# Kernel tuning notes

Measured on AMD Instinct MI355X. Metric: run time of the kernel, lower is better.

## Reference

```python
import jax, jax.numpy as jnp
import numpy as np

B_GRAPHS = 16      # number of graphs in batch
NPG = 8192         # nodes per graph
N = B_GRAPHS * NPG # 131072 total nodes
F_DIM = 64         # node feature dim
K_CLUST = 16       # n_clusters
DEG = 32           # avg degree
E = N * DEG        # 4,194,304 edges


def setup_inputs() -> dict:
    key = jax.random.key(0)
    k1, k2, k3, k4, k5 = jax.random.split(key, 5)
    x = jax.random.normal(k1, (N, F_DIM), jnp.float32)
    W = jax.random.normal(k2, (F_DIM, K_CLUST), jnp.float32) / np.sqrt(F_DIM)
    b = jnp.zeros((K_CLUST,), jnp.float32)
    # edges constrained within each graph -> block-diagonal adjacency (PyG batching)
    g = jnp.repeat(jnp.arange(B_GRAPHS, dtype=jnp.int32), E // B_GRAPHS)
    edge_row = g * NPG + jax.random.randint(k3, (E,), 0, NPG, jnp.int32)
    edge_col = g * NPG + jax.random.randint(k4, (E,), 0, NPG, jnp.int32)
    edge_weight = jax.random.uniform(k5, (E,), jnp.float32)
    return {"x": x, "W": W, "b": b, "edge_weight": edge_weight,
            "edge_row": edge_row, "edge_col": edge_col, "num_graphs": B_GRAPHS}


def _forward(x, W, b, edge_weight, edge_row, edge_col, num_graphs):
    Ntot, Fd = x.shape
    K = W.shape[1]
    Bn = num_graphs
    n = Ntot // Bn  # equal-size graphs (ptr = n * arange(B+1))

    s = x @ W + b                                   # [N,K] cluster logits
    xb = x.reshape(Bn, n, Fd)
    sb = s.reshape(Bn, n, K)
    # out_x = selu(s^T @ x_bd), block b = s_b^T x_b, then hsplit_and_vstack -> [B*K, F]
    out_x = jax.nn.selu(jnp.einsum('bnk,bnf->bkf', sb, xb)).reshape(Bn * K, Fd)

    ss = jax.nn.softmax(s, axis=-1)                 # softmaxed assignments
    ssb = ss.reshape(Bn, n, K)

    # degree d = adj.sum(axis=0)  (column sums over COO edges)
    d = jax.ops.segment_sum(edge_weight, edge_col, num_segments=Ntot)   # [N]
    m2 = d.reshape(Bn, n).sum(1)                    # total degree per graph [B]

    # A @ C via edge scatter: (A C)[row] += w * C[col]
    AC = jax.ops.segment_sum(edge_weight[:, None] * ss[edge_col], edge_row,
                             num_segments=Ntot)     # [N,K]
    # out_adj blocks: C_b^T A_b C_b  -> [B,K,K]
    out_adj = jnp.einsum('bnk,bnl->bkl', ssb, AC.reshape(Bn, n, K))

    # dS_b = C_b^T d_b  (Ca/Cb blocks); normalizer gets m_inv twice in torch code
    dS = jnp.einsum('bn,bnk->bk', d.reshape(Bn, n), ssb)                # [B,K]
    spectral_loss = -jnp.mean(jnp.einsum('bkk->b', out_adj) / m2
                              - (dS ** 2).sum(1) / (m2 ** 2))

    sqrt_K = jnp.sqrt(jnp.float32(K))
    cluster_size = ssb.sum(1)                        # [B,K]
    cluster_loss = jnp.mean(jnp.sqrt((cluster_size ** 2).sum(1)) / n * sqrt_K - 1.0)

    # CC blocks: C_b^T C_b; ortho = mean_b || CC_b/||CC_b||_F - I/sqrt(K) ||_F
    CC = jnp.einsum('bnk,bnl->bkl', ssb, ssb)        # [B,K,K]
    CC_norm = jnp.sqrt((CC ** 2).sum((1, 2)))        # Frobenius norm per block
    eye_div_k = jnp.eye(K, dtype=x.dtype) / sqrt_K
    ortho_loss = jnp.mean(jnp.sqrt(
        ((CC / CC_norm[:, None, None] - eye_div_k) ** 2).sum((1, 2))))

    # mask diagonal and degree-normalize pooled adjacency
    oa = out_adj * (1.0 - jnp.eye(K, dtype=x.dtype))
    dd = jnp.sqrt(oa.sum(2)) + 1e-12                 # row sums per block [B,K]
    out_adj_norm = oa / (dd[:, :, None] * dd[:, None, :])

    return out_x, out_adj_norm, spectral_loss, cluster_loss, ortho_loss


def reference(x, W, b, edge_weight, edge_row, edge_col, num_graphs):
    return _forward(x, W, b, edge_weight, edge_row, edge_col, num_graphs)
```

## Files before the change

### kernel.cpp

```cpp
#include <hip/hip_runtime.h>
#include <math.h>

#define F_DIM 64
#define K_CL 16
#define B_GR 16
#define SROW 72

typedef _Float16 h16;
using f16x4 = __attribute__((ext_vector_type(4))) _Float16;
using f16x8 = __attribute__((ext_vector_type(8))) _Float16;
using f32x4 = __attribute__((ext_vector_type(4))) float;
using fx2   = __attribute__((ext_vector_type(2))) float;
using fp16x2 = __attribute__((ext_vector_type(2))) __fp16;

static __device__ inline unsigned h2u(fp16x2 h) {
    union { fp16x2 h; unsigned u; } x; x.h = h; return x.u;
}

__global__ __launch_bounds__(256) void k_fused(
    const float* __restrict__ x, const float* __restrict__ W, const float* __restrict__ bvec,
    uint4* __restrict__ ssh8, float* __restrict__ outx, float* __restrict__ CCb)
{
    __shared__ float Wl[F_DIM * K_CL];
    __shared__ float bl[K_CL];
    __shared__ __align__(16) h16 stage[4][(16 + 16 + 64) * SROW];

    int t = threadIdx.x;
    for (int idx = t; idx < F_DIM * K_CL; idx += 256) Wl[idx] = W[idx];
    if (t < K_CL) bl[t] = bvec[t];
    __syncthreads();

    int wid = t >> 6, lane = t & 63;
    h16* Sg = stage[wid];
    h16* Cg = Sg + 16 * SROW;
    h16* Xg = Cg + 16 * SROW;

    size_t i = (size_t)blockIdx.x * 256 + t;
    float s[16];
#pragma unroll
    for (int k = 0; k < 16; ++k) s[k] = bl[k];

    const float4* xp = reinterpret_cast<const float4*>(x + i * F_DIM);
#pragma unroll
    for (int j = 0; j < 16; ++j) {
        float4 q = xp[j];
        float xf[4] = {q.x, q.y, q.z, q.w};
#pragma unroll
        for (int ff = 0; ff < 4; ++ff) {
            int f = j * 4 + ff;
            float xv = xf[ff];
            Xg[f * SROW + lane] = (h16)xv;
            const float4* wr = reinterpret_cast<const float4*>(&Wl[f * K_CL]);
            float4 w0 = wr[0], w1 = wr[1], w2 = wr[2], w3 = wr[3];
            s[0]  += xv * w0.x; s[1]  += xv * w0.y; s[2]  += xv * w0.z; s[3]  += xv * w0.w;
            s[4]  += xv * w1.x; s[5]  += xv * w1.y; s[6]  += xv * w1.z; s[7]  += xv * w1.w;
            s[8]  += xv * w2.x; s[9]  += xv * w2.y; s[10] += xv * w2.z; s[11] += xv * w2.w;
            s[12] += xv * w3.x; s[13] += xv * w3.y; s[14] += xv * w3.z; s[15] += xv * w3.w;
        }
    }

#pragma unroll
    for (int k = 0; k < 16; ++k) Sg[k * SROW + lane] = (h16)s[k];

    float m = s[0];
#pragma unroll
    for (int k = 1; k < 16; ++k) m = fmaxf(m, s[k]);
    float sum = 0.f;
#pragma unroll
    for (int k = 0; k < 16; ++k) { s[k] = __expf(s[k] - m); sum += s[k]; }
    float inv = 1.0f / sum;
#pragma unroll
    for (int k = 0; k < 16; ++k) s[k] *= inv;

    f16x8 h0, h1;
#pragma unroll
    for (int k = 0; k < 8; ++k) { h0[k] = (h16)s[k]; h1[k] = (h16)s[k + 8]; }
#pragma unroll
    for (int k = 0; k < 8; ++k) {
        Cg[k * SROW + lane] = h0[k];
        Cg[(k + 8) * SROW + lane] = h1[k];
    }

    {
        unsigned d0, d1, d2, d3;
        d0 = __builtin_amdgcn_cvt_pk_fp8_f32(s[0],  s[1],  0,  false);
        d0 = __builtin_amdgcn_cvt_pk_fp8_f32(s[2],  s[3],  d0, true);
        d1 = __builtin_amdgcn_cvt_pk_fp8_f32(s[4],  s[5],  0,  false);
        d1 = __builtin_amdgcn_cvt_pk_fp8_f32(s[6],  s[7],  d1, true);
        d2 = __builtin_amdgcn_cvt_pk_fp8_f32(s[8],  s[9],  0,  false);
        d2 = __builtin_amdgcn_cvt_pk_fp8_f32(s[10], s[11], d2, true);
        d3 = __builtin_amdgcn_cvt_pk_fp8_f32(s[12], s[13], 0,  false);
        d3 = __builtin_amdgcn_cvt_pk_fp8_f32(s[14], s[15], d3, true);
        uint4 pk; pk.x = d0; pk.y = d1; pk.z = d2; pk.w = d3;
        ssh8[i] = pk;
    }

    int q4 = lane >> 4, mm = lane & 15;
    f32x4 accO[4] = {{0.f,0.f,0.f,0.f},{0.f,0.f,0.f,0.f},{0.f,0.f,0.f,0.f},{0.f,0.f,0.f,0.f}};
    f32x4 accC = {0.f, 0.f, 0.f, 0.f};
#pragma unroll
    for (int h = 0; h < 2; ++h) {
        f16x8 aO = *(const f16x8*)&Sg[mm * SROW + h * 32 + q4 * 8];
        f16x8 aC = *(const f16x8*)&Cg[mm * SROW + h * 32 + q4 * 8];
        accC = __builtin_amdgcn_mfma_f32_16x16x32_f16(aC, aC, accC, 0, 0, 0);
#pragma unroll
        for (int ft = 0; ft < 4; ++ft) {
            f16x8 bO = *(const f16x8*)&Xg[(ft * 16 + mm) * SROW + h * 32 + q4 * 8];
            accO[ft] = __builtin_amdgcn_mfma_f32_16x16x32_f16(aO, bO, accO[ft], 0, 0, 0);
        }
    }
    __syncthreads();

    float* redO = (float*)&stage[0][0];
    float* redC = redO + 4096;
#pragma unroll
    for (int ft = 0; ft < 4; ++ft)
#pragma unroll
        for (int rg = 0; rg < 4; ++rg)
            redO[wid * 1024 + (q4 * 4 + rg) * 64 + ft * 16 + mm] = accO[ft][rg];
#pragma unroll
    for (int rg = 0; rg < 4; ++rg)
        redC[wid * 256 + (q4 * 4 + rg) * 16 + mm] = accC[rg];
    __syncthreads();

    int g = blockIdx.x >> 5;
#pragma unroll
    for (int it = 0; it < 4; ++it) {
        int idx = t + it * 256;
        float v = redO[idx] + redO[1024 + idx] + redO[2048 + idx] + redO[3072 + idx];
        atomicAdd(outx + g * 1024 + idx, v);
    }
    {
        float v = redC[t] + redC[256 + t] + redC[512 + t] + redC[768 + t];
        atomicAdd(CCb + g * 256 + t, v);
    }
}

__global__ __launch_bounds__(256) void k_edge(
    const int* __restrict__ erow, const int* __restrict__ ecol, const float* __restrict__ ew,
    const uint4* __restrict__ ssh8, float* __restrict__ oadj,
    int edges_per_block, int edges_per_graph, int nmask)
{
    __shared__ float CCl[256];
    __shared__ __align__(16) h16 stageE[4][2048];
    int t = threadIdx.x;
    CCl[t] = 0.f;
    __syncthreads();

    int bid = blockIdx.x;
    int xcd = bid & 7;
    int slot = bid >> 3;
    int graph = xcd + 8 * (slot & 1);
    int chunk = slot >> 1;

    int wid = t >> 6, lane = t & 63;
    int q4 = lane >> 4, mm = lane & 15;
    h16* Ag = stageE[wid];

    int epw = edges_per_block >> 2;
    int nt  = epw >> 6;
    size_t base = (size_t)graph * edges_per_graph
                + (size_t)chunk * edges_per_block
                + (size_t)wid * epw
                + lane;

    f32x4 acc = {0.f, 0.f, 0.f, 0.f};

    f16x8* Aw = reinterpret_cast<f16x8*>(Ag);
    using lds_h16 = __attribute__((address_space(3))) h16;
    unsigned trA = (unsigned)(uintptr_t)(lds_h16*)Ag + (unsigned)(q4 * 256 + mm * 2);

    auto dec_dw = [](unsigned d, float w, unsigned& o0, unsigned& o1) {
        fx2 p = __builtin_amdgcn_cvt_pk_f32_fp8((int)d, false);
        fx2 q = __builtin_amdgcn_cvt_pk_f32_fp8((int)d, true);
        o0 = h2u(__builtin_amdgcn_cvt_pkrtz(p.x * w, p.y * w));
        o1 = h2u(__builtin_amdgcn_cvt_pkrtz(q.x * w, q.y * w));
    };

    auto compute_tile = [&](uint4 va, uint4 vb, float wv) {
        union { unsigned u[4]; f16x8 v; } alo, ahi, blo, bhi;
        dec_dw(va.x, wv, alo.u[0], alo.u[1]);
        dec_dw(va.y, wv, alo.u[2], alo.u[3]);
        dec_dw(va.z, wv, ahi.u[0], ahi.u[1]);
        dec_dw(va.w, wv, ahi.u[2], ahi.u[3]);
        dec_dw(vb.x, 1.0f, blo.u[0], blo.u[1]);
        dec_dw(vb.y, 1.0f, blo.u[2], blo.u[3]);
        dec_dw(vb.z, 1.0f, bhi.u[0], bhi.u[1]);
        dec_dw(vb.w, 1.0f, bhi.u[2], bhi.u[3]);

        Aw[lane * 2]           = alo.v;
        Aw[lane * 2 + 1]       = ahi.v;
        Aw[128 + lane * 2]     = blo.v;
        Aw[128 + lane * 2 + 1] = bhi.v;

        f16x4 xa0, xa1, xa2, xa3, xb0, xb1, xb2, xb3;
        asm volatile(
            "ds_read_b64_tr_b16 %0, %8\n\t"
            "ds_read_b64_tr_b16 %1, %8 offset:128\n\t"
            "ds_read_b64_tr_b16 %2, %8 offset:2048\n\t"
            "ds_read_b64_tr_b16 %3, %8 offset:2176\n\t"
            "ds_read_b64_tr_b16 %4, %8 offset:1024\n\t"
            "ds_read_b64_tr_b16 %5, %8 offset:1152\n\t"
            "ds_read_b64_tr_b16 %6, %8 offset:3072\n\t"
            "ds_read_b64_tr_b16 %7, %8 offset:3200\n\t"
            "s_waitcnt lgkmcnt(0)"
            : "=&v"(xa0), "=&v"(xa1), "=&v"(xb0), "=&v"(xb1),
              "=&v"(xa2), "=&v"(xa3), "=&v"(xb2), "=&v"(xb3)
            : "v"(trA)
            : "memory");
        __builtin_amdgcn_sched_barrier(0);

        f16x8 afL = __builtin_shufflevector(xa0, xa1, 0, 1, 2, 3, 4, 5, 6, 7);
        f16x8 bfL = __builtin_shufflevector(xb0, xb1, 0, 1, 2, 3, 4, 5, 6, 7);
        f16x8 afH = __builtin_shufflevector(xa2, xa3, 0, 1, 2, 3, 4, 5, 6, 7);
        f16x8 bfH = __builtin_shufflevector(xb2, xb3, 0, 1, 2, 3, 4, 5, 6, 7);
        acc = __builtin_amdgcn_mfma_f32_16x16x32_f16(afL, bfL, acc, 0, 0, 0);
        acc = __builtin_amdgcn_mfma_f32_16x16x32_f16(afH, bfH, acc, 0, 0, 0);
    };

    int rC, cC; float wC;
    rC = erow[base]; cC = ecol[base]; wC = ew[base];
    uint4 ca = ssh8[(size_t)(rC & nmask)];
    uint4 cb = ssh8[(size_t)(cC & nmask)];
    int rN = 0, cN = 0; float wN = 0.f;
    {
        size_t e = base + 64;
        rN = erow[e]; cN = ecol[e]; wN = ew[e];
    }

    for (int tt = 0; tt < nt - 1; ++tt) {
        uint4 na = ssh8[(size_t)(rN & nmask)];
        uint4 nb = ssh8[(size_t)(cN & nmask)];
        int t2 = (tt + 2 < nt) ? (tt + 2) : 0;
        size_t e2 = base + (size_t)t2 * 64;
        int r2 = erow[e2], c2 = ecol[e2];
        float w2 = ew[e2];

        compute_tile(ca, cb, wC);

        ca = na; cb = nb; wC = wN;
        rN = r2; cN = c2; wN = w2;
    }
    compute_tile(ca, cb, wC);

#pragma unroll
    for (int rg = 0; rg < 4; ++rg)
        atomicAdd(&CCl[(q4 * 4 + rg) * 16 + mm], acc[rg]);
    __syncthreads();
    atomicAdd(oadj + graph * 256 + t, CCl[t]);
}

__global__ __launch_bounds__(256) void k_final(
    const float* __restrict__ outx, const float* __restrict__ oadj,
    const float* __restrict__ CCb, float* __restrict__ out, int npg)
{
    int t = threadIdx.x;
    int gid = blockIdx.x * 256 + t;
    {
        float v = outx[gid];
        float r = (v > 0.f) ? (1.0507009873554805f * v)
                            : (1.0507009873554805f * 1.6732632423543772f * (__expf(v) - 1.0f));
        out[gid] = r;
    }

    if (blockIdx.x != 0) return;

    int b = t >> 4, k = t & 15;
    const float* oar = oadj + b * 256 + k * 16;
    const float* ccr = CCb + b * 256 + k * 16;

    float rowsum_off = 0.f, trace_c = 0.f, rowsum_all = 0.f, fro2 = 0.f, colsum = 0.f;
    float csv = 0.f;
#pragma unroll
    for (int l = 0; l < 16; ++l) {
        float v = oar[l];
        rowsum_all += v;
        if (l == k) trace_c = v; else rowsum_off += v;
        float c = ccr[l];
        fro2 += c * c;
        csv += c;
        colsum += oadj[b * 256 + l * 16 + k];
    }
    float dd = sqrtf(rowsum_off) + 1e-12f;
    __shared__ float ddl[B_GR * K_CL];
    ddl[t] = dd;

    float ds2 = colsum * colsum, cs2 = csv * csv;
    float tr = trace_c, m2 = rowsum_all;
#pragma unroll
    for (int msk = 8; msk >= 1; msk >>= 1) {
        tr   += __shfl_xor(tr,   msk, 16);
        ds2  += __shfl_xor(ds2,  msk, 16);
        cs2  += __shfl_xor(cs2,  msk, 16);
        fro2 += __shfl_xor(fro2, msk, 16);
        m2   += __shfl_xor(m2,   msk, 16);
    }
    float invfro = 1.0f / sqrtf(fro2);
    float osum = 0.f;
#pragma unroll
    for (int l = 0; l < 16; ++l) {
        float v = ccr[l] * invfro - ((l == k) ? 0.25f : 0.f);
        osum += v * v;
    }
#pragma unroll
    for (int msk = 8; msk >= 1; msk >>= 1) osum += __shfl_xor(osum, msk, 16);

    __shared__ float sp_s[B_GR], cl_s[B_GR], or_s[B_GR];
    if (k == 0) {
        sp_s[b] = tr / m2 - ds2 / (m2 * m2);
        cl_s[b] = sqrtf(cs2) / (float)npg * 4.0f - 1.0f;
        or_s[b] = sqrtf(osum);
    }
    __syncthreads();
    if (t == 0) {
        float a = 0.f, c = 0.f, o = 0.f;
        for (int i = 0; i < B_GR; ++i) { a += sp_s[i]; c += cl_s[i]; o += or_s[i]; }
        out[20480] = -a / 16.f;
        out[20481] = c / 16.f;
        out[20482] = o / 16.f;
    }

#pragma unroll
    for (int l = 0; l < 16; ++l) {
        float v = (l == k) ? 0.f : oar[l] / (dd * ddl[b * 16 + l]);
        out[16384 + b * 256 + k * 16 + l] = v;
    }
}

extern "C" void kernel_launch(void* const* d_in, const int* in_sizes, int n_in,
                              void* d_out, int out_size, void* d_ws, size_t ws_size,
                              hipStream_t stream)
{
    const float* x    = (const float*)d_in[0];
    const float* W    = (const float*)d_in[1];
    const float* bvec = (const float*)d_in[2];
    const float* ew   = (const float*)d_in[3];
    const int* erow   = (const int*)d_in[4];
    const int* ecol   = (const int*)d_in[5];

    int Ntot = in_sizes[0] / F_DIM;
    size_t E = (size_t)in_sizes[3];
    int npg  = Ntot / B_GR;
    int edges_per_graph = (int)(E / B_GR);
    int nmask = Ntot - 1;

    const int ADJ_BLOCKS = 2048;
    int edges_per_block = (int)(E / ADJ_BLOCKS);

    char* ws = (char*)d_ws;
    size_t o = 0;
    uint4* ssh8  = (uint4*)(ws + o); o += (size_t)Ntot * 16;
    size_t zoff = o;
    float* outx  = (float*)(ws + o); o += (size_t)B_GR * 1024 * 4;
    float* oadj  = (float*)(ws + o); o += (size_t)B_GR * 256 * 4;
    float* CCb   = (float*)(ws + o); o += (size_t)B_GR * 256 * 4;

    (void)hipMemsetAsync(ws + zoff, 0, o - zoff, stream);

    k_fused<<<Ntot / 256, 256, 0, stream>>>(x, W, bvec, ssh8, outx, CCb);
    k_edge<<<ADJ_BLOCKS, 256, 0, stream>>>(erow, ecol, ew, ssh8, oadj,
                                           edges_per_block, edges_per_graph, nmask);
    k_final<<<64, 256, 0, stream>>>(outx, oadj, CCb, (float*)d_out, npg);
}
```

Before: 173.1 us.

## Fold memset and finalize kernel into fused/edge kernels via last-block ticket

Removes the hipMemsetAsync and the separate k_final launch. k_fused now zeroes oadj and the ticket and writes per-block partials instead of using global atomics. k_edge blocks reduce those partials (selu out_x, CCb) before their edge work, and the last block to finish, chosen by an atomic ticket, computes the losses and normalized adjacency. This saves two launches and avoids atomic contention, but adds a serial tail in the last block and extra partial-buffer traffic.

```diff
diff --git a/kernel.cpp b/kernel.cpp
--- a/kernel.cpp
+++ b/kernel.cpp
@@ -19,13 +19,20 @@
 
 __global__ __launch_bounds__(256) void k_fused(
     const float* __restrict__ x, const float* __restrict__ W, const float* __restrict__ bvec,
-    uint4* __restrict__ ssh8, float* __restrict__ outx, float* __restrict__ CCb)
+    uint4* __restrict__ ssh8, float* __restrict__ outxP, float* __restrict__ CCbP,
+    float* __restrict__ oadj, unsigned* __restrict__ ticket)
 {
     __shared__ float Wl[F_DIM * K_CL];
     __shared__ float bl[K_CL];
     __shared__ __align__(16) h16 stage[4][(16 + 16 + 64) * SROW];
 
     int t = threadIdx.x;
+    int bid = blockIdx.x;
+    if (bid == 0) {
+#pragma unroll
+        for (int i = 0; i < 16; ++i) oadj[t + i * 256] = 0.f;
+        if (t == 0) *ticket = 0u;
+    }
     for (int idx = t; idx < F_DIM * K_CL; idx += 256) Wl[idx] = W[idx];
     if (t < K_CL) bl[t] = bvec[t];
     __syncthreads();
@@ -35,7 +42,7 @@
     h16* Cg = Sg + 16 * SROW;
     h16* Xg = Cg + 16 * SROW;
 
-    size_t i = (size_t)blockIdx.x * 256 + t;
+    size_t i = (size_t)bid * 256 + t;
     float s[16];
 #pragma unroll
     for (int k = 0; k < 16; ++k) s[k] = bl[k];
@@ -123,26 +130,31 @@
         redC[wid * 256 + (q4 * 4 + rg) * 16 + mm] = accC[rg];
     __syncthreads();
 
-    int g = blockIdx.x >> 5;
 #pragma unroll
     for (int it = 0; it < 4; ++it) {
         int idx = t + it * 256;
         float v = redO[idx] + redO[1024 + idx] + redO[2048 + idx] + redO[3072 + idx];
-        atomicAdd(outx + g * 1024 + idx, v);
+        outxP[(size_t)bid * 1024 + idx] = v;
     }
     {
         float v = redC[t] + redC[256 + t] + redC[512 + t] + redC[768 + t];
-        atomicAdd(CCb + g * 256 + t, v);
+        CCbP[(size_t)bid * 256 + t] = v;
     }
 }
 
 __global__ __launch_bounds__(256) void k_edge(
     const int* __restrict__ erow, const int* __restrict__ ecol, const float* __restrict__ ew,
     const uint4* __restrict__ ssh8, float* __restrict__ oadj,
-    int edges_per_block, int edges_per_graph, int nmask)
+    const float* __restrict__ outxP, const float* __restrict__ CCbP,
+    float* __restrict__ CCb, float* __restrict__ out, unsigned* __restrict__ ticket,
+    int edges_per_block, int edges_per_graph, int nmask, int npg, int nblocks)
 {
     __shared__ float CCl[256];
     __shared__ __align__(16) h16 stageE[4][2048];
+    __shared__ float ddl[256];
+    __shared__ float sp_s[B_GR], cl_s[B_GR], or_s[B_GR];
+    __shared__ unsigned elect;
+
     int t = threadIdx.x;
     CCl[t] = 0.f;
     __syncthreads();
@@ -152,6 +164,23 @@
     int slot = bid >> 3;
     int graph = xcd + 8 * (slot & 1);
     int chunk = slot >> 1;
+
+    if (chunk < 32) {
+        if (t < 32) {
+            int idx = chunk * 32 + t;
+            float sv = 0.f;
+            for (int sub = 0; sub < 32; ++sub)
+                sv += outxP[(size_t)(graph * 32 + sub) * 1024 + idx];
+            float r = (sv > 0.f) ? (1.0507009873554805f * sv)
+                                 : (1.0507009873554805f * 1.6732632423543772f * (__expf(sv) - 1.0f));
+            out[graph * 1024 + idx] = r;
+        }
+    } else if (chunk == 32) {
+        float sv = 0.f;
+        for (int sub = 0; sub < 32; ++sub)
+            sv += CCbP[(size_t)(graph * 32 + sub) * 256 + t];
+        atomicExch(CCb + graph * 256 + t, sv);
+    }
 
     int wid = t >> 6, lane = t & 63;
     int q4 = lane >> 4, mm = lane & 15;
@@ -248,82 +277,80 @@
         atomicAdd(&CCl[(q4 * 4 + rg) * 16 + mm], acc[rg]);
     __syncthreads();
     atomicAdd(oadj + graph * 256 + t, CCl[t]);
-}
-
-__global__ __launch_bounds__(256) void k_final(
-    const float* __restrict__ outx, const float* __restrict__ oadj,
-    const float* __restrict__ CCb, float* __restrict__ out, int npg)
-{
-    int t = threadIdx.x;
-    int gid = blockIdx.x * 256 + t;
+
+    __threadfence();
+    __syncthreads();
+    if (t == 0) elect = atomicAdd(ticket, 1u);
+    __syncthreads();
+    if (elect != (unsigned)(nblocks - 1)) return;
+
     {
-        float v = outx[gid];
-        float r = (v > 0.f) ? (1.0507009873554805f * v)
-                            : (1.0507009873554805f * 1.6732632423543772f * (__expf(v) - 1.0f));
-        out[gid] = r;
-    }
-
-    if (blockIdx.x != 0) return;
-
-    int b = t >> 4, k = t & 15;
-    const float* oar = oadj + b * 256 + k * 16;
-    const float* ccr = CCb + b * 256 + k * 16;
-
-    float rowsum_off = 0.f, trace_c = 0.f, rowsum_all = 0.f, fro2 = 0.f, colsum = 0.f;
-    float csv = 0.f;
-#pragma unroll
-    for (int l = 0; l < 16; ++l) {
-        float v = oar[l];
-        rowsum_all += v;
-        if (l == k) trace_c = v; else rowsum_off += v;
-        float c = ccr[l];
-        fro2 += c * c;
-        csv += c;
-        colsum += oadj[b * 256 + l * 16 + k];
-    }
-    float dd = sqrtf(rowsum_off) + 1e-12f;
-    __shared__ float ddl[B_GR * K_CL];
-    ddl[t] = dd;
-
-    float ds2 = colsum * colsum, cs2 = csv * csv;
-    float tr = trace_c, m2 = rowsum_all;
-#pragma unroll
-    for (int msk = 8; msk >= 1; msk >>= 1) {
-        tr   += __shfl_xor(tr,   msk, 16);
-        ds2  += __shfl_xor(ds2,  msk, 16);
-        cs2  += __shfl_xor(cs2,  msk, 16);
-        fro2 += __shfl_xor(fro2, msk, 16);
-        m2   += __shfl_xor(m2,   msk, 16);
-    }
-    float invfro = 1.0f / sqrtf(fro2);
-    float osum = 0.f;
-#pragma unroll
-    for (int l = 0; l < 16; ++l) {
-        float v = ccr[l] * invfro - ((l == k) ? 0.25f : 0.f);
-        osum += v * v;
-    }
-#pragma unroll
-    for (int msk = 8; msk >= 1; msk >>= 1) osum += __shfl_xor(osum, msk, 16);
-
-    __shared__ float sp_s[B_GR], cl_s[B_GR], or_s[B_GR];
-    if (k == 0) {
-        sp_s[b] = tr / m2 - ds2 / (m2 * m2);
-        cl_s[b] = sqrtf(cs2) / (float)npg * 4.0f - 1.0f;
-        or_s[b] = sqrtf(osum);
-    }
-    __syncthreads();
-    if (t == 0) {
-        float a = 0.f, c = 0.f, o = 0.f;
-        for (int i = 0; i < B_GR; ++i) { a += sp_s[i]; c += cl_s[i]; o += or_s[i]; }
-        out[20480] = -a / 16.f;
-        out[20481] = c / 16.f;
-        out[20482] = o / 16.f;
-    }
-
-#pragma unroll
-    for (int l = 0; l < 16; ++l) {
-        float v = (l == k) ? 0.f : oar[l] / (dd * ddl[b * 16 + l]);
-        out[16384 + b * 256 + k * 16 + l] = v;
+        int b = t >> 4, k = t & 15;
+        float* oabase = oadj + b * 256;
+        float* ccbase = CCb + b * 256;
+
+        float oar[16], ocol[16], ccr[16];
+#pragma unroll
+        for (int l = 0; l < 16; ++l) {
+            oar[l]  = atomicAdd(&oabase[k * 16 + l], 0.f);
+            ocol[l] = atomicAdd(&oabase[l * 16 + k], 0.f);
+            ccr[l]  = atomicAdd(&ccbase[k * 16 + l], 0.f);
+        }
+
+        float rowsum_off = 0.f, trace_c = 0.f, rowsum_all = 0.f, fro2 = 0.f;
+        float colsum = 0.f, csv = 0.f;
+#pragma unroll
+        for (int l = 0; l < 16; ++l) {
+            float v = oar[l];
+            rowsum_all += v;
+            if (l == k) trace_c = v; else rowsum_off += v;
+            float c = ccr[l];
+            fro2 += c * c;
+            csv += c;
+            colsum += ocol[l];
+        }
+        float dd = sqrtf(rowsum_off) + 1e-12f;
+        ddl[t] = dd;
+
+        float ds2 = colsum * colsum, cs2 = csv * csv;
+        float tr = trace_c, m2 = rowsum_all;
+#pragma unroll
+        for (int msk = 8; msk >= 1; msk >>= 1) {
+            tr   += __shfl_xor(tr,   msk, 16);
+            ds2  += __shfl_xor(ds2,  msk, 16);
+            cs2  += __shfl_xor(cs2,  msk, 16);
+            fro2 += __shfl_xor(fro2, msk, 16);
+            m2   += __shfl_xor(m2,   msk, 16);
+        }
+        float invfro = 1.0f / sqrtf(fro2);
+        float osum = 0.f;
+#pragma unroll
+        for (int l = 0; l < 16; ++l) {
+            float v = ccr[l] * invfro - ((l == k) ? 0.25f : 0.f);
+            osum += v * v;
+        }
+#pragma unroll
+        for (int msk = 8; msk >= 1; msk >>= 1) osum += __shfl_xor(osum, msk, 16);
+
+        if (k == 0) {
+            sp_s[b] = tr / m2 - ds2 / (m2 * m2);
+            cl_s[b] = sqrtf(cs2) / (float)npg * 4.0f - 1.0f;
+            or_s[b] = sqrtf(osum);
+        }
+        __syncthreads();
+        if (t == 0) {
+            float a = 0.f, c = 0.f, o = 0.f;
+            for (int i2 = 0; i2 < B_GR; ++i2) { a += sp_s[i2]; c += cl_s[i2]; o += or_s[i2]; }
+            out[20480] = -a / 16.f;
+            out[20481] = c / 16.f;
+            out[20482] = o / 16.f;
+        }
+
+#pragma unroll
+        for (int l = 0; l < 16; ++l) {
+            float v = (l == k) ? 0.f : oar[l] / (dd * ddl[b * 16 + l]);
+            out[16384 + b * 256 + k * 16 + l] = v;
+        }
     }
 }
 
@@ -343,22 +370,23 @@
     int npg  = Ntot / B_GR;
     int edges_per_graph = (int)(E / B_GR);
     int nmask = Ntot - 1;
+    int nfb   = Ntot / 256;
 
     const int ADJ_BLOCKS = 2048;
     int edges_per_block = (int)(E / ADJ_BLOCKS);
 
     char* ws = (char*)d_ws;
     size_t o = 0;
-    uint4* ssh8  = (uint4*)(ws + o); o += (size_t)Ntot * 16;
-    size_t zoff = o;
-    float* outx  = (float*)(ws + o); o += (size_t)B_GR * 1024 * 4;
-    float* oadj  = (float*)(ws + o); o += (size_t)B_GR * 256 * 4;
-    float* CCb   = (float*)(ws + o); o += (size_t)B_GR * 256 * 4;
-
-    (void)hipMemsetAsync(ws + zoff, 0, o - zoff, stream);
-
-    k_fused<<<Ntot / 256, 256, 0, stream>>>(x, W, bvec, ssh8, outx, CCb);
+    uint4* ssh8  = (uint4*)(ws + o);    o += (size_t)Ntot * 16;
+    float* outxP = (float*)(ws + o);    o += (size_t)nfb * 1024 * 4;
+    float* CCbP  = (float*)(ws + o);    o += (size_t)nfb * 256 * 4;
+    float* oadj  = (float*)(ws + o);    o += (size_t)B_GR * 256 * 4;
+    float* CCb   = (float*)(ws + o);    o += (size_t)B_GR * 256 * 4;
+    unsigned* ticket = (unsigned*)(ws + o); o += 64;
+
+    k_fused<<<nfb, 256, 0, stream>>>(x, W, bvec, ssh8, outxP, CCbP, oadj, ticket);
     k_edge<<<ADJ_BLOCKS, 256, 0, stream>>>(erow, ecol, ew, ssh8, oadj,
-                                           edges_per_block, edges_per_graph, nmask);
-    k_final<<<64, 256, 0, stream>>>(outx, oadj, CCb, (float*)d_out, npg);
+                                           outxP, CCbP, CCb, (float*)d_out, ticket,
+                                           edges_per_block, edges_per_graph, nmask,
+                                           npg, ADJ_BLOCKS);
 }
```

Result: slower. 351.5 us (+103.0%).
